# Performance work log

Hardware: AMD Instinct MI355X
Metric: run time of the kernel (lower is better)

The kernel has to match this reference:

```python
import jax, jax.numpy as jnp
import numpy as np

N_VERTS = 40962  # icosphere level-6 vertex count
K_RING = 19      # 2-ring filter size


def setup_inputs() -> dict:
    key = jax.random.key(0)
    k1, k2, k3, k4 = jax.random.split(key, 4)
    B, C_in, C_out = 4, 64, 64
    x = jax.random.normal(k1, (B, C_in, N_VERTS), dtype=jnp.float32)
    neigh_orders = jax.random.randint(k2, (N_VERTS, K_RING), 0, N_VERTS, dtype=jnp.int32)
    # nn.Linear(19*in_feats, out_feats): weight [C_out, 19*C_in], bias [C_out]
    fan_in = K_RING * C_in
    bound = 1.0 / np.sqrt(fan_in)
    W = jax.random.uniform(k3, (C_out, fan_in), dtype=jnp.float32, minval=-bound, maxval=bound)
    b = jax.random.uniform(k4, (C_out,), dtype=jnp.float32, minval=-bound, maxval=bound)
    return {"x": x, "neigh_orders": neigh_orders, "W": W, "b": b}


def reference(x, neigh_orders, W, b):
    # x: [B, C_in, N] -> [B, N, C_in]
    xt = jnp.transpose(x, (0, 2, 1))
    B, N, C = xt.shape
    # gather 19-ring neighbors: [B, N, 19, C_in]
    gathered = xt[:, neigh_orders, :]
    # im2col-style flatten: [B, N, 19*C_in]
    mat = gathered.reshape(B, N, K_RING * C)
    # Linear: mat @ W.T + b -> [B, N, C_out]
    out = jnp.einsum('bnk,ok->bno', mat, W) + b
    # back to [B, C_out, N]
    return jnp.transpose(out, (0, 2, 1))
```

## Files before the change

### kernel.cpp

```cpp
#include <hip/hip_runtime.h>
#include <hip/hip_bf16.h>


#define NV   40962
#define KR   19
#define CIN  64
#define COUT 64
#define NB   4
#define NTILES 321

typedef __bf16 bf16;
typedef __bf16 bf16x8 __attribute__((ext_vector_type(8)));
typedef float  floatx4 __attribute__((ext_vector_type(4)));

#define XT_ELEMS ((size_t)NB * NV * CIN)
#define WB_OFF   ((XT_ELEMS * 2 + 255) & ~(size_t)255)
#define WS_NEED  (WB_OFF + (size_t)COUT * KR * CIN * 2)

__global__ __launch_bounds__(256) void transpose_kernel(
    const float* __restrict__ x, bf16* __restrict__ xt)
{
    __shared__ float tile[64 * 65];
    const int b  = blockIdx.y;
    const int v0 = blockIdx.x * 64;
    const int t  = threadIdx.x;

    const int vl = t & 63;
    const int c0 = t >> 6;
    const int vg = min(v0 + vl, NV - 1);
    #pragma unroll
    for (int p = 0; p < 16; ++p) {
        int c = c0 * 16 + p;
        tile[vl * 65 + c] = x[((size_t)(b * CIN + c)) * NV + vg];
    }
    __syncthreads();

    const int v = t >> 2;
    const int q = t & 3;
    if (v0 + v < NV) {
        #pragma unroll
        for (int p = 0; p < 2; ++p) {
            int chunk = q + p * 4;
            bf16x8 o;
            #pragma unroll
            for (int j = 0; j < 8; ++j)
                o[j] = (bf16)tile[v * 65 + chunk * 8 + j];
            *(bf16x8*)&xt[((size_t)(b * NV + v0 + v)) * 64 + chunk * 8] = o;
        }
    }
}

__global__ __launch_bounds__(256) void convw_kernel(
    const float* __restrict__ W, bf16* __restrict__ Wb)
{
    int i = blockIdx.x * 256 + threadIdx.x;
    const int total4 = COUT * KR * CIN / 4;
    if (i < total4) {
        float4 v = ((const float4*)W)[i];
        bf16* p = Wb + (size_t)i * 4;
        p[0] = (bf16)v.x; p[1] = (bf16)v.y; p[2] = (bf16)v.z; p[3] = (bf16)v.w;
    }
}

__global__ __launch_bounds__(256, 4) void conv_kernel(
    const int*   __restrict__ neigh,
    const bf16*  __restrict__ xt,
    const bf16*  __restrict__ Wb,
    const float* __restrict__ bias,
    float*       __restrict__ out)
{
    __shared__ alignas(16) bf16 Wlds[2][64 * 72];

    const int i    = blockIdx.x;
    const int b    = (i & 7) >> 1;
    const int tile = (i >> 3) * 2 + (i & 1);
    if (tile >= NTILES) return;
    const int n0   = tile * 128;

    const int t    = threadIdx.x;
    const int wv   = t >> 6;
    const int lane = t & 63;
    const int l15  = lane & 15;
    const int g    = lane >> 4;

    int nn[2], ib[2];
    #pragma unroll
    for (int s = 0; s < 2; ++s) {
        nn[s] = n0 + wv * 32 + s * 16 + l15;
        ib[s] = min(nn[s], NV - 1) * KR;
    }

    floatx4 acc[2][4];
    #pragma unroll
    for (int s = 0; s < 2; ++s)
        #pragma unroll
        for (int o = 0; o < 4; ++o)
            acc[s][o] = (floatx4){0.f, 0.f, 0.f, 0.f};

    const int wo = t >> 2;
    const int wc = t & 3;

    #pragma unroll
    for (int p2 = 0; p2 < 2; ++p2) {
        int chunk = wc + p2 * 4;
        *(bf16x8*)&Wlds[0][wo * 72 + chunk * 8] =
            *(const bf16x8*)&Wb[(size_t)wo * (KR * 64) + chunk * 8];
    }
    bf16x8 xfc[2][2], xfn[2][2];
    #pragma unroll
    for (int s = 0; s < 2; ++s) {
        int v = neigh[ib[s]];
        v = ((unsigned)v < (unsigned)NV) ? v : 0;
        const bf16* p = xt + (((size_t)(b * NV + v)) << 6) + g * 8;
        xfc[s][0] = *(const bf16x8*)(p);
        xfc[s][1] = *(const bf16x8*)(p + 32);
    }
    __syncthreads();

    for (int r = 0; r < KR; ++r) {
        if (r + 1 < KR) {
            #pragma unroll
            for (int s = 0; s < 2; ++s) {
                int v = neigh[ib[s] + r + 1];
                v = ((unsigned)v < (unsigned)NV) ? v : 0;
                const bf16* p = xt + (((size_t)(b * NV + v)) << 6) + g * 8;
                xfn[s][0] = *(const bf16x8*)(p);
                xfn[s][1] = *(const bf16x8*)(p + 32);
            }
            #pragma unroll
            for (int p2 = 0; p2 < 2; ++p2) {
                int chunk = wc + p2 * 4;
                *(bf16x8*)&Wlds[(r + 1) & 1][wo * 72 + chunk * 8] =
                    *(const bf16x8*)&Wb[(size_t)wo * (KR * 64) + (r + 1) * 64 + chunk * 8];
            }
        }

        #pragma unroll
        for (int ot = 0; ot < 4; ++ot) {
            #pragma unroll
            for (int kc = 0; kc < 2; ++kc) {
                bf16x8 wf = *(const bf16x8*)
                    &Wlds[r & 1][(ot * 16 + l15) * 72 + kc * 32 + g * 8];
                #pragma unroll
                for (int s = 0; s < 2; ++s) {
                    acc[s][ot] = __builtin_amdgcn_mfma_f32_16x16x32_bf16(
                        wf, xfc[s][kc], acc[s][ot], 0, 0, 0);
                }
            }
        }
        __syncthreads();
        #pragma unroll
        for (int s = 0; s < 2; ++s) {
            xfc[s][0] = xfn[s][0];
            xfc[s][1] = xfn[s][1];
        }
    }

    #pragma unroll
    for (int ot = 0; ot < 4; ++ot) {
        #pragma unroll
        for (int ii = 0; ii < 4; ++ii) {
            int o = ot * 16 + g * 4 + ii;
            float bv = bias[o];
            #pragma unroll
            for (int s = 0; s < 2; ++s) {
                if (nn[s] < NV) {
                    out[((size_t)(b * COUT + o)) * NV + nn[s]] =
                        acc[s][ot][ii] + bv;
                }
            }
        }
    }
}

__global__ __launch_bounds__(64) void fallback_kernel(
    const int*   __restrict__ neigh,
    const float* __restrict__ x,
    const float* __restrict__ W,
    const float* __restrict__ bias,
    float*       __restrict__ out)
{
    __shared__ float xg[KR * CIN];
    const int bn = blockIdx.x;
    const int b  = bn / NV;
    const int n  = bn % NV;
    const int t  = threadIdx.x;

    for (int k = t; k < KR * CIN; k += 64) {
        int r = k / CIN, c = k - r * CIN;
        int v = neigh[n * KR + r];
        v = ((unsigned)v < (unsigned)NV) ? v : 0;
        xg[k] = x[((size_t)(b * CIN + c)) * NV + v];
    }
    __syncthreads();

    float s = bias[t];
    const float* wrow = W + (size_t)t * (KR * CIN);
    for (int k = 0; k < KR * CIN; ++k) s += xg[k] * wrow[k];
    out[((size_t)(b * COUT + t)) * NV + n] = s;
}

extern "C" void kernel_launch(void* const* d_in, const int* in_sizes, int n_in,
                              void* d_out, int out_size, void* d_ws, size_t ws_size,
                              hipStream_t stream)
{
    const float* x     = (const float*)d_in[0];
    const int*   neigh = (const int*)d_in[1];
    const float* W     = (const float*)d_in[2];
    const float* bias  = (const float*)d_in[3];
    float* out = (float*)d_out;

    if (d_ws != nullptr && ws_size >= WS_NEED) {
        bf16* xt = (bf16*)d_ws;
        bf16* Wb = (bf16*)((char*)d_ws + WB_OFF);

        dim3 tgrid((NV + 63) / 64, NB);
        transpose_kernel<<<tgrid, 256, 0, stream>>>(x, xt);
        convw_kernel<<<(COUT * KR * CIN / 4 + 255) / 256, 256, 0, stream>>>(W, Wb);

        int nblk = 8 * ((NTILES + 1) / 2);
        conv_kernel<<<nblk, 256, 0, stream>>>(neigh, xt, Wb, bias, out);
    } else {
        fallback_kernel<<<NB * NV, 64, 0, stream>>>(neigh, x, W, bias, out);
    }
}
```

Measured before the change: 170.2 us.

## Load weight fragments directly into registers and deepen gather prefetch to two stages

Removes the shared-memory double buffer for weights and the per-iteration block barrier; each lane now loads its MFMA weight fragments straight from global memory (L2/L1-resident) into registers, prefetching one ring ahead. The neighbor-feature gather is deepened from one-ahead to two-ahead prefetch, and the ring loop is fully unrolled. Occupancy hint is lowered from 4 to 3 blocks per CU to allow more registers. It trades redundant global weight loads across waves for fewer barriers and more latency hiding on the irregular gathers.

New measurement: 259.0 us. 52.2% more time.

```diff
diff --git a/kernel.cpp b/kernel.cpp
--- a/kernel.cpp
+++ b/kernel.cpp
@@ -62,15 +62,13 @@
     }
 }
 
-__global__ __launch_bounds__(256, 4) void conv_kernel(
+__global__ __launch_bounds__(256, 3) void conv_kernel(
     const int*   __restrict__ neigh,
     const bf16*  __restrict__ xt,
     const bf16*  __restrict__ Wb,
     const float* __restrict__ bias,
     float*       __restrict__ out)
 {
-    __shared__ alignas(16) bf16 Wlds[2][64 * 72];
-
     const int i    = blockIdx.x;
     const int b    = (i & 7) >> 1;
     const int tile = (i >> 3) * 2 + (i & 1);
@@ -90,6 +88,9 @@
         ib[s] = min(nn[s], NV - 1) * KR;
     }
 
+    const bf16* xb = xt + (((size_t)b * NV) << 6) + g * 8;
+    const bf16* wp = Wb + (size_t)l15 * (KR * 64) + g * 8;
+
     floatx4 acc[2][4];
     #pragma unroll
     for (int s = 0; s < 2; ++s)
@@ -97,63 +98,71 @@
         for (int o = 0; o < 4; ++o)
             acc[s][o] = (floatx4){0.f, 0.f, 0.f, 0.f};
 
-    const int wo = t >> 2;
-    const int wc = t & 3;
-
-    #pragma unroll
-    for (int p2 = 0; p2 < 2; ++p2) {
-        int chunk = wc + p2 * 4;
-        *(bf16x8*)&Wlds[0][wo * 72 + chunk * 8] =
-            *(const bf16x8*)&Wb[(size_t)wo * (KR * 64) + chunk * 8];
-    }
-    bf16x8 xfc[2][2], xfn[2][2];
-    #pragma unroll
-    for (int s = 0; s < 2; ++s) {
-        int v = neigh[ib[s]];
-        v = ((unsigned)v < (unsigned)NV) ? v : 0;
-        const bf16* p = xt + (((size_t)(b * NV + v)) << 6) + g * 8;
-        xfc[s][0] = *(const bf16x8*)(p);
-        xfc[s][1] = *(const bf16x8*)(p + 32);
-    }
-    __syncthreads();
-
+    bf16x8 xf[2][2][2];
+    bf16x8 wf[4][2];
+
+    #pragma unroll
+    for (int pr = 0; pr < 2; ++pr) {
+        #pragma unroll
+        for (int s = 0; s < 2; ++s) {
+            int v = neigh[ib[s] + pr];
+            v = ((unsigned)v < (unsigned)NV) ? v : 0;
+            const bf16* p = xb + ((size_t)v << 6);
+            xf[pr][s][0] = *(const bf16x8*)(p);
+            xf[pr][s][1] = *(const bf16x8*)(p + 32);
+        }
+    }
+    #pragma unroll
+    for (int ot = 0; ot < 4; ++ot)
+        #pragma unroll
+        for (int kc = 0; kc < 2; ++kc)
+            wf[ot][kc] = *(const bf16x8*)
+                (wp + (size_t)(ot * 16) * (KR * 64) + kc * 32);
+
+    #pragma unroll
     for (int r = 0; r < KR; ++r) {
+        const int st = r & 1;
+
+        bf16x8 c[2][2];
+        #pragma unroll
+        for (int s = 0; s < 2; ++s) {
+            c[s][0] = xf[st][s][0];
+            c[s][1] = xf[st][s][1];
+        }
+        bf16x8 w[4][2];
+        #pragma unroll
+        for (int ot = 0; ot < 4; ++ot) {
+            w[ot][0] = wf[ot][0];
+            w[ot][1] = wf[ot][1];
+        }
+
+        if (r + 2 < KR) {
+            #pragma unroll
+            for (int s = 0; s < 2; ++s) {
+                int v = neigh[ib[s] + r + 2];
+                v = ((unsigned)v < (unsigned)NV) ? v : 0;
+                const bf16* p = xb + ((size_t)v << 6);
+                xf[st][s][0] = *(const bf16x8*)(p);
+                xf[st][s][1] = *(const bf16x8*)(p + 32);
+            }
+        }
         if (r + 1 < KR) {
             #pragma unroll
-            for (int s = 0; s < 2; ++s) {
-                int v = neigh[ib[s] + r + 1];
-                v = ((unsigned)v < (unsigned)NV) ? v : 0;
-                const bf16* p = xt + (((size_t)(b * NV + v)) << 6) + g * 8;
-                xfn[s][0] = *(const bf16x8*)(p);
-                xfn[s][1] = *(const bf16x8*)(p + 32);
-            }
-            #pragma unroll
-            for (int p2 = 0; p2 < 2; ++p2) {
-                int chunk = wc + p2 * 4;
-                *(bf16x8*)&Wlds[(r + 1) & 1][wo * 72 + chunk * 8] =
-                    *(const bf16x8*)&Wb[(size_t)wo * (KR * 64) + (r + 1) * 64 + chunk * 8];
-            }
-        }
-
-        #pragma unroll
-        for (int ot = 0; ot < 4; ++ot) {
-            #pragma unroll
-            for (int kc = 0; kc < 2; ++kc) {
-                bf16x8 wf = *(const bf16x8*)
-                    &Wlds[r & 1][(ot * 16 + l15) * 72 + kc * 32 + g * 8];
+            for (int ot = 0; ot < 4; ++ot)
                 #pragma unroll
-                for (int s = 0; s < 2; ++s) {
+                for (int kc = 0; kc < 2; ++kc)
+                    wf[ot][kc] = *(const bf16x8*)
+                        (wp + (size_t)(ot * 16) * (KR * 64) + (r + 1) * 64 + kc * 32);
+        }
+
+        #pragma unroll
+        for (int ot = 0; ot < 4; ++ot)
+            #pragma unroll
+            for (int kc = 0; kc < 2; ++kc)
+                #pragma unroll
+                for (int s = 0; s < 2; ++s)
                     acc[s][ot] = __builtin_amdgcn_mfma_f32_16x16x32_bf16(
-                        wf, xfc[s][kc], acc[s][ot], 0, 0, 0);
-                }
-            }
-        }
-        __syncthreads();
-        #pragma unroll
-        for (int s = 0; s < 2; ++s) {
-            xfc[s][0] = xfn[s][0];
-            xfc[s][1] = xfn[s][1];
-        }
+                        w[ot][kc], c[s][kc], acc[s][ot], 0, 0, 0);
     }
 
     #pragma unroll
```

## Process two rings per barrier with fragment-ordered LDS weight layout

Applied to the files above, without the earlier changes.

Restructures the conv main loop to handle two ring offsets per iteration, halving the number of __syncthreads barriers and doubling the neighbor gathers and weight tiles in flight per prefetch stage. The LDS weight tile is stored pre-swizzled in MFMA fragment order, so each lane reads a contiguous 16-byte chunk indexed by lane instead of a padded row-major layout. The loop is fully unrolled. This raises register and LDS usage, which may reduce occupancy under the 256x4 launch bound.

Result: no change. 169.5 us (-0.4%).

```diff
diff --git a/kernel.cpp b/kernel.cpp
--- a/kernel.cpp
+++ b/kernel.cpp
@@ -69,7 +69,7 @@
     const float* __restrict__ bias,
     float*       __restrict__ out)
 {
-    __shared__ alignas(16) bf16 Wlds[2][64 * 72];
+    __shared__ alignas(16) bf16 Wlds[2][2][4096];
 
     const int i    = blockIdx.x;
     const int b    = (i & 7) >> 1;
@@ -90,6 +90,17 @@
         ib[s] = min(nn[s], NV - 1) * KR;
     }
 
+    const bf16* xb = xt + (((size_t)b * NV) << 6) + g * 8;
+
+    const int srow = t >> 2;
+    const int c4   = t & 3;
+    const int skc  = c4 >> 1;
+    const int sg0  = (c4 & 1) * 2;
+    const int sot  = srow >> 4, sl15 = srow & 15;
+    const int sdst0 = ((sot * 2 + skc) * 64 + (sg0 + 0) * 16 + sl15) * 8;
+    const int sdst1 = ((sot * 2 + skc) * 64 + (sg0 + 1) * 16 + sl15) * 8;
+    const bf16* sw = Wb + (size_t)srow * (KR * 64) + c4 * 16;
+
     floatx4 acc[2][4];
     #pragma unroll
     for (int s = 0; s < 2; ++s)
@@ -97,63 +108,79 @@
         for (int o = 0; o < 4; ++o)
             acc[s][o] = (floatx4){0.f, 0.f, 0.f, 0.f};
 
-    const int wo = t >> 2;
-    const int wc = t & 3;
-
-    #pragma unroll
-    for (int p2 = 0; p2 < 2; ++p2) {
-        int chunk = wc + p2 * 4;
-        *(bf16x8*)&Wlds[0][wo * 72 + chunk * 8] =
-            *(const bf16x8*)&Wb[(size_t)wo * (KR * 64) + chunk * 8];
-    }
-    bf16x8 xfc[2][2], xfn[2][2];
-    #pragma unroll
-    for (int s = 0; s < 2; ++s) {
-        int v = neigh[ib[s]];
-        v = ((unsigned)v < (unsigned)NV) ? v : 0;
-        const bf16* p = xt + (((size_t)(b * NV + v)) << 6) + g * 8;
-        xfc[s][0] = *(const bf16x8*)(p);
-        xfc[s][1] = *(const bf16x8*)(p + 32);
+    bf16x8 xf[2][2][2];
+    bf16x8 xg[2][2][2];
+
+    #pragma unroll
+    for (int j = 0; j < 2; ++j) {
+        bf16x8 w0 = *(const bf16x8*)(sw + j * 64);
+        bf16x8 w1 = *(const bf16x8*)(sw + j * 64 + 8);
+        *(bf16x8*)(&Wlds[0][j][sdst0]) = w0;
+        *(bf16x8*)(&Wlds[0][j][sdst1]) = w1;
+        #pragma unroll
+        for (int s = 0; s < 2; ++s) {
+            int v = neigh[ib[s] + j];
+            v = ((unsigned)v < (unsigned)NV) ? v : 0;
+            const bf16* p = xb + ((size_t)v << 6);
+            xf[j][s][0] = *(const bf16x8*)(p);
+            xf[j][s][1] = *(const bf16x8*)(p + 32);
+        }
     }
     __syncthreads();
 
-    for (int r = 0; r < KR; ++r) {
-        if (r + 1 < KR) {
+    #pragma unroll
+    for (int rp = 0; rp < 10; ++rp) {
+        const int st = rp & 1;
+
+        if (rp + 1 < 10) {
+            #pragma unroll
+            for (int j = 0; j < 2; ++j) {
+                const int ring = 2 * (rp + 1) + j;
+                if (ring < KR) {
+                    bf16x8 w0 = *(const bf16x8*)(sw + ring * 64);
+                    bf16x8 w1 = *(const bf16x8*)(sw + ring * 64 + 8);
+                    *(bf16x8*)(&Wlds[st ^ 1][j][sdst0]) = w0;
+                    *(bf16x8*)(&Wlds[st ^ 1][j][sdst1]) = w1;
+                    #pragma unroll
+                    for (int s = 0; s < 2; ++s) {
+                        int v = neigh[ib[s] + ring];
+                        v = ((unsigned)v < (unsigned)NV) ? v : 0;
+                        const bf16* p = xb + ((size_t)v << 6);
+                        xg[j][s][0] = *(const bf16x8*)(p);
+                        xg[j][s][1] = *(const bf16x8*)(p + 32);
+                    }
+                }
+            }
+        }
+
+        #pragma unroll
+        for (int j = 0; j < 2; ++j) {
+            const int ring = 2 * rp + j;
+            if (ring < KR) {
+                const bf16* wbase = &Wlds[st][j][lane * 8];
+                #pragma unroll
+                for (int ot = 0; ot < 4; ++ot) {
+                    #pragma unroll
+                    for (int kc = 0; kc < 2; ++kc) {
+                        bf16x8 wf = *(const bf16x8*)(wbase + (ot * 2 + kc) * 512);
+                        #pragma unroll
+                        for (int s = 0; s < 2; ++s) {
+                            acc[s][ot] = __builtin_amdgcn_mfma_f32_16x16x32_bf16(
+                                wf, xf[j][s][kc], acc[s][ot], 0, 0, 0);
+                        }
+                    }
+                }
+            }
+        }
+        __syncthreads();
+
+        #pragma unroll
+        for (int j = 0; j < 2; ++j)
             #pragma unroll
             for (int s = 0; s < 2; ++s) {
-                int v = neigh[ib[s] + r + 1];
-                v = ((unsigned)v < (unsigned)NV) ? v : 0;
-                const bf16* p = xt + (((size_t)(b * NV + v)) << 6) + g * 8;
-                xfn[s][0] = *(const bf16x8*)(p);
-                xfn[s][1] = *(const bf16x8*)(p + 32);
-            }
-            #pragma unroll
-            for (int p2 = 0; p2 < 2; ++p2) {
-                int chunk = wc + p2 * 4;
-                *(bf16x8*)&Wlds[(r + 1) & 1][wo * 72 + chunk * 8] =
-                    *(const bf16x8*)&Wb[(size_t)wo * (KR * 64) + (r + 1) * 64 + chunk * 8];
-            }
-        }
-
-        #pragma unroll
-        for (int ot = 0; ot < 4; ++ot) {
-            #pragma unroll
-            for (int kc = 0; kc < 2; ++kc) {
-                bf16x8 wf = *(const bf16x8*)
-                    &Wlds[r & 1][(ot * 16 + l15) * 72 + kc * 32 + g * 8];
-                #pragma unroll
-                for (int s = 0; s < 2; ++s) {
-                    acc[s][ot] = __builtin_amdgcn_mfma_f32_16x16x32_bf16(
-                        wf, xfc[s][kc], acc[s][ot], 0, 0, 0);
-                }
-            }
-        }
-        __syncthreads();
-        #pragma unroll
-        for (int s = 0; s < 2; ++s) {
-            xfc[s][0] = xfn[s][0];
-            xfc[s][1] = xfn[s][1];
-        }
+                xf[j][s][0] = xg[j][s][0];
+                xf[j][s][1] = xg[j][s][1];
+            }
     }
 
     #pragma unroll
```
